# Performance work log

Hardware: AMD Instinct MI355X
Metric: run time of the kernel (lower is better)

The kernel has to match this reference:

```python
import jax, jax.numpy as jnp
import numpy as np

B, C, N = 16, 128, 2048  # batch, channels (SA_Layer(128)), num points


def setup_inputs() -> dict:
    key = jax.random.key(0)
    ks = jax.random.split(key, 6)
    x = jax.random.normal(ks[0], (B, C, N), jnp.float32)
    wq = jax.random.normal(ks[1], (C // 4, C), jnp.float32) * 0.05  # shared q/k 1x1 conv, no bias
    wv = jax.random.normal(ks[2], (C, C), jnp.float32) * 0.05
    bv = jax.random.normal(ks[3], (C,), jnp.float32) * 0.05
    wt = jax.random.normal(ks[4], (C, C), jnp.float32) * 0.05
    bt = jax.random.normal(ks[5], (C,), jnp.float32) * 0.05
    gamma = jnp.ones((C,), jnp.float32)   # BatchNorm1d weight
    beta = jnp.zeros((C,), jnp.float32)   # BatchNorm1d bias
    bn_mean = jnp.zeros((C,), jnp.float32)  # running mean (eval mode)
    bn_var = jnp.ones((C,), jnp.float32)    # running var (eval mode)
    return dict(x=x, wq=wq, wv=wv, bv=bv, wt=wt, bt=bt,
                gamma=gamma, beta=beta, bn_mean=bn_mean, bn_var=bn_var)


def reference(x, wq, wv, bv, wt, bt, gamma, beta, bn_mean, bn_var):
    EPS = 1e-9
    BN_EPS = 1e-5
    # q_conv and k_conv share weights (tied in __init__)
    x_q = jnp.einsum('dc,bcn->bnd', wq, x)               # [B, N, C/4]
    x_k = jnp.einsum('dc,bcn->bdn', wq, x)               # [B, C/4, N]
    energy = jnp.einsum('bnd,bdm->bnm', x_q, x_k)        # [B, N, N]
    attn = jax.nn.softmax(energy, axis=-1)
    # offset-attention renormalization: divide by column sum
    attn = attn / (EPS + attn.sum(axis=1, keepdims=True))
    x_v = jnp.einsum('dc,bcn->bdn', wv, x) + bv[None, :, None]   # [B, C, N]
    x_r = jnp.einsum('bdn,bnm->bdm', x_v, attn)                  # [B, C, N]
    t = jnp.einsum('dc,bcn->bdn', wt, x - x_r) + bt[None, :, None]
    # BatchNorm1d (eval mode) + ReLU
    t = (t - bn_mean[None, :, None]) * jax.lax.rsqrt(bn_var + BN_EPS)[None, :, None]
    t = t * gamma[None, :, None] + beta[None, :, None]
    return x + jax.nn.relu(t)
```

## Files before the change

kernel.cpp:

```cpp
#include <hip/hip_runtime.h>
#include <hip/hip_bf16.h>
#include <math.h>

#define BB 16
#define CC 128
#define NN 2048
#define CQ 32

typedef __attribute__((ext_vector_type(8))) short bf16x8;
typedef __attribute__((ext_vector_type(4))) float f32x4;
typedef __attribute__((ext_vector_type(16))) float f32x16;

__device__ __forceinline__ ushort f2b(float f) {
    __hip_bfloat16 h = __float2bfloat16(f);
    return *reinterpret_cast<ushort*>(&h);
}
__device__ __forceinline__ float b2f(ushort u) {
    union { unsigned u; float f; } v; v.u = ((unsigned)u) << 16;
    return v.f;
}
__device__ __forceinline__ bf16x8 as_b8(uint4 u) {
    union { uint4 u; bf16x8 b; } v; v.u = u; return v.b;
}
__device__ __forceinline__ float fexp2(float x) {
    return __builtin_amdgcn_exp2f(x);
}

#define OFF_VB  524288
#define OFF_XRB 2621440
#define OFF_RSI 4718592

#define QSCALE 1.2011224087864498f

__global__ __launch_bounds__(256) void k_proj(const float* __restrict__ x,
        const float* __restrict__ wq, const float* __restrict__ wv,
        const float* __restrict__ bv, ushort* __restrict__ Qt, ushort* __restrict__ Vb) {
    __shared__ ushort Wl[160][136];
    __shared__ ushort Xs[64][136];
    int bid = (blockIdx.x & 7) * 64 + (blockIdx.x >> 3);
    int b  = bid >> 5;
    int n0 = (bid & 31) << 6;
    int tid = threadIdx.x;
    #pragma unroll
    for (int k = 0; k < 20; ++k) {
        int idx = k * 256 + tid;
        int r = idx >> 5, c4 = (idx & 31) << 2;
        const float* srcw = (r < 32) ? (wq + r * 128 + c4) : (wv + (r - 32) * 128 + c4);
        float4 w4 = *(const float4*)srcw;
        float s = (r < 32) ? QSCALE : 1.0f;
        *(ushort4*)&Wl[r][c4] = make_ushort4(f2b(w4.x * s), f2b(w4.y * s),
                                             f2b(w4.z * s), f2b(w4.w * s));
    }
    const float* xb = x + (size_t)b * CC * NN;
    for (int idx = tid; idx < 2048; idx += 256) {
        int c = idx >> 4, n4 = (idx & 15) << 2;
        float4 xv = *(const float4*)&xb[c * NN + n0 + n4];
        Xs[n4][c]     = f2b(xv.x);
        Xs[n4 + 1][c] = f2b(xv.y);
        Xs[n4 + 2][c] = f2b(xv.z);
        Xs[n4 + 3][c] = f2b(xv.w);
    }
    __syncthreads();
    int w = tid >> 6, l = tid & 63, lr = l & 15, lg = l >> 4;
    f32x4 zero = {0.f, 0.f, 0.f, 0.f};
    int nn = n0 + w * 16 + lr;
    for (int dt = 0; dt < 10; ++dt) {
        f32x4 acc = zero;
        #pragma unroll
        for (int k = 0; k < 4; ++k) {
            bf16x8 a  = *(const bf16x8*)&Wl[dt * 16 + lr][k * 32 + lg * 8];
            bf16x8 bx = *(const bf16x8*)&Xs[w * 16 + lr][k * 32 + lg * 8];
            acc = __builtin_amdgcn_mfma_f32_16x16x32_bf16(a, bx, acc, 0, 0, 0);
        }
        if (dt < 2) {
            ushort4 p = make_ushort4(f2b(acc[0]), f2b(acc[1]), f2b(acc[2]), f2b(acc[3]));
            *(ushort4*)&Qt[(size_t)(b * NN + nn) * CQ + dt * 16 + lg * 4] = p;
        } else {
            #pragma unroll
            for (int i = 0; i < 4; ++i) {
                int vd = (dt - 2) * 16 + lg * 4 + i;
                Vb[(size_t)(b * CC + vd) * NN + nn] = f2b(acc[i] + bv[vd]);
            }
        }
    }
}

__global__ __launch_bounds__(512) void k_rowstats(const ushort* __restrict__ Qt,
        float* __restrict__ RSI) {
    __shared__ ushort Qm[128][36];
    __shared__ float Sred[2][64];
    int bid = (blockIdx.x & 7) * 64 + (blockIdx.x >> 3);
    int b  = bid >> 5;
    int n0 = (bid & 31) << 6;
    int tid = threadIdx.x;
    int w = tid >> 6, l = tid & 63, lr = l & 15, lg = l >> 4;
    int wn = w & 3, wm = w >> 2;
    const ushort* Qtb = Qt + (size_t)b * NN * CQ;
    bf16x8 aq = *(const bf16x8*)&Qtb[(size_t)(n0 + wn * 16 + lr) * CQ + lg * 8];
    int sr = tid >> 2, sc = (tid & 3) * 8;
    uint4 q0 = *(const uint4*)&Qtb[(size_t)sr * CQ + sc];
    float S[4] = {0.f, 0.f, 0.f, 0.f};
    f32x4 zero = {0.f, 0.f, 0.f, 0.f};
    for (int t = 0; t < 16; ++t) {
        __syncthreads();
        *(uint4*)&Qm[sr][sc] = q0;
        __syncthreads();
        if (t < 15)
            q0 = *(const uint4*)&Qtb[(size_t)((t + 1) * 128 + sr) * CQ + sc];
        #pragma unroll
        for (int mi = 0; mi < 4; ++mi) {
            bf16x8 bq = *(const bf16x8*)&Qm[(wm * 4 + mi) * 16 + lr][lg * 8];
            f32x4 e = __builtin_amdgcn_mfma_f32_16x16x32_bf16(aq, bq, zero, 0, 0, 0);
            S[0] += fexp2(e[0]); S[1] += fexp2(e[1]);
            S[2] += fexp2(e[2]); S[3] += fexp2(e[3]);
        }
    }
    #pragma unroll
    for (int d = 1; d < 16; d <<= 1) {
        #pragma unroll
        for (int i = 0; i < 4; ++i) S[i] += __shfl_xor(S[i], d);
    }
    if (lr == 0) {
        #pragma unroll
        for (int i = 0; i < 4; ++i) Sred[wm][wn * 16 + lg * 4 + i] = S[i];
    }
    __syncthreads();
    if (tid < 64)
        RSI[b * NN + n0 + tid] = 1.f / (Sred[0][tid] + Sred[1][tid]);
}

__global__ __launch_bounds__(768, 3) void k_attn_pv(const ushort* __restrict__ Qt,
        const ushort* __restrict__ Vb, const float* __restrict__ RSI,
        ushort* __restrict__ XRb) {
    __shared__ ushort Vs[2][128][68];
    __shared__ ushort Ws[2][128][68];
    __shared__ float csred[4][128];
    __shared__ float csum[128];
    int bid = (blockIdx.x & 7) * 32 + (blockIdx.x >> 3);
    int b  = bid >> 4;
    int m0 = (bid & 15) << 7;
    int tid = threadIdx.x;
    int w = tid >> 6, l = tid & 63, lr = l & 15, lg = l >> 4;
    const ushort* Qtb = Qt + (size_t)b * NN * CQ;
    const ushort* Vbb = Vb + (size_t)b * CC * NN;
    const float*  RSb = RSI + (size_t)b * NN;
    f32x4 zero = {0.f, 0.f, 0.f, 0.f};
    bool producer = (w < 8);

    int wn = w & 3, mh = w >> 2;
    bf16x8 bm[4];
    float cs[4] = {0.f, 0.f, 0.f, 0.f};
    int sv = 0, shv = 0;
    const ushort* vsrc = nullptr;
    bf16x8 aq_nx; float4 rsi_nx;
    int cw = w - 8;
    int dh = cw >> 1, mh2 = cw & 1;
    int ar = l & 31, kh = l >> 5;
    f32x16 pacc00, pacc01, pacc10, pacc11;

    if (producer) {
        #pragma unroll
        for (int mi = 0; mi < 4; ++mi)
            bm[mi] = *(const bf16x8*)&Qtb[(size_t)(m0 + (mh * 4 + mi) * 16 + lr) * CQ + lg * 8];
        sv = tid >> 2; shv = (tid & 3) * 16;
        vsrc = Vbb + (size_t)sv * NN + shv;
        {
            uint4 v0 = *(const uint4*)(vsrc);
            uint4 v1 = *(const uint4*)(vsrc + 8);
            ushort* dst = &Vs[0][sv][shv];
            *(uint2*)(dst)      = make_uint2(v0.x, v0.y);
            *(uint2*)(dst + 4)  = make_uint2(v0.z, v0.w);
            *(uint2*)(dst + 8)  = make_uint2(v1.x, v1.y);
            *(uint2*)(dst + 12) = make_uint2(v1.z, v1.w);
        }
        {
            bf16x8 aq0 = *(const bf16x8*)&Qtb[(size_t)(wn * 16 + lr) * CQ + lg * 8];
            float4 r4 = *(const float4*)&RSb[wn * 16 + lg * 4];
            int nb = wn * 16 + lg * 4;
            #pragma unroll
            for (int mi = 0; mi < 4; ++mi) {
                f32x4 e = __builtin_amdgcn_mfma_f32_16x16x32_bf16(aq0, bm[mi], zero, 0, 0, 0);
                float w0 = fexp2(e[0]) * r4.x;
                float w1 = fexp2(e[1]) * r4.y;
                float w2 = fexp2(e[2]) * r4.z;
                float w3 = fexp2(e[3]) * r4.w;
                cs[mi] += w0 + w1 + w2 + w3;
                *(ushort4*)&Ws[0][(mh * 4 + mi) * 16 + lr][nb] =
                    make_ushort4(f2b(w0), f2b(w1), f2b(w2), f2b(w3));
            }
        }
        aq_nx  = *(const bf16x8*)&Qtb[(size_t)(64 + wn * 16 + lr) * CQ + lg * 8];
        rsi_nx = *(const float4*)&RSb[64 + wn * 16 + lg * 4];
    } else {
        #pragma unroll
        for (int r = 0; r < 16; ++r) {
            pacc00[r] = 0.f; pacc01[r] = 0.f; pacc10[r] = 0.f; pacc11[r] = 0.f;
        }
    }
    __syncthreads();
    for (int t = 0; t < 32; ++t) {
        int cur = t & 1;
        if (producer) {
            if (t < 31) {
                int ntn = (t + 1) * 64;
                uint4 v0 = *(const uint4*)(vsrc + ntn);
                uint4 v1 = *(const uint4*)(vsrc + ntn + 8);
                bf16x8 aq = aq_nx;
                float4 r4 = rsi_nx;
                if (t < 30) {
                    int nt2 = (t + 2) * 64;
                    aq_nx  = *(const bf16x8*)&Qtb[(size_t)(nt2 + wn * 16 + lr) * CQ + lg * 8];
                    rsi_nx = *(const float4*)&RSb[nt2 + wn * 16 + lg * 4];
                }
                int nb = wn * 16 + lg * 4;
                #pragma unroll
                for (int mi = 0; mi < 4; ++mi) {
                    f32x4 e = __builtin_amdgcn_mfma_f32_16x16x32_bf16(aq, bm[mi], zero, 0, 0, 0);
                    float w0 = fexp2(e[0]) * r4.x;
                    float w1 = fexp2(e[1]) * r4.y;
                    float w2 = fexp2(e[2]) * r4.z;
                    float w3 = fexp2(e[3]) * r4.w;
                    cs[mi] += w0 + w1 + w2 + w3;
                    *(ushort4*)&Ws[cur ^ 1][(mh * 4 + mi) * 16 + lr][nb] =
                        make_ushort4(f2b(w0), f2b(w1), f2b(w2), f2b(w3));
                }
                ushort* dst = &Vs[cur ^ 1][sv][shv];
                *(uint2*)(dst)      = make_uint2(v0.x, v0.y);
                *(uint2*)(dst + 4)  = make_uint2(v0.z, v0.w);
                *(uint2*)(dst + 8)  = make_uint2(v1.x, v1.y);
                *(uint2*)(dst + 12) = make_uint2(v1.z, v1.w);
            }
        } else {
            __builtin_amdgcn_s_setprio(1);
            #pragma unroll
            for (int kk = 0; kk < 4; ++kk) {
                const ushort* vp0 = &Vs[cur][dh * 64 + ar][kk * 16 + kh * 8];
                const ushort* vp1 = &Vs[cur][dh * 64 + 32 + ar][kk * 16 + kh * 8];
                uint2 a0 = *(const uint2*)vp0; uint2 a1 = *(const uint2*)(vp0 + 4);
                uint2 a2 = *(const uint2*)vp1; uint2 a3 = *(const uint2*)(vp1 + 4);
                bf16x8 va0 = as_b8(make_uint4(a0.x, a0.y, a1.x, a1.y));
                bf16x8 va1 = as_b8(make_uint4(a2.x, a2.y, a3.x, a3.y));
                const ushort* wp0 = &Ws[cur][mh2 * 64 + ar][kk * 16 + kh * 8];
                const ushort* wp1 = &Ws[cur][mh2 * 64 + 32 + ar][kk * 16 + kh * 8];
                uint2 b0 = *(const uint2*)wp0; uint2 b1 = *(const uint2*)(wp0 + 4);
                uint2 c0 = *(const uint2*)wp1; uint2 c1 = *(const uint2*)(wp1 + 4);
                bf16x8 wb0 = as_b8(make_uint4(b0.x, b0.y, b1.x, b1.y));
                bf16x8 wb1 = as_b8(make_uint4(c0.x, c0.y, c1.x, c1.y));
                pacc00 = __builtin_amdgcn_mfma_f32_32x32x16_bf16(va0, wb0, pacc00, 0, 0, 0);
                pacc01 = __builtin_amdgcn_mfma_f32_32x32x16_bf16(va0, wb1, pacc01, 0, 0, 0);
                pacc10 = __builtin_amdgcn_mfma_f32_32x32x16_bf16(va1, wb0, pacc10, 0, 0, 0);
                pacc11 = __builtin_amdgcn_mfma_f32_32x32x16_bf16(va1, wb1, pacc11, 0, 0, 0);
            }
            __builtin_amdgcn_s_setprio(0);
        }
        __syncthreads();
    }
    if (producer) {
        #pragma unroll
        for (int mi = 0; mi < 4; ++mi) {
            cs[mi] += __shfl_xor(cs[mi], 16);
            cs[mi] += __shfl_xor(cs[mi], 32);
        }
        if (lg == 0) {
            #pragma unroll
            for (int mi = 0; mi < 4; ++mi)
                csred[wn][(mh * 4 + mi) * 16 + lr] = cs[mi];
        }
    }
    __syncthreads();
    if (tid < 128) {
        float tot = csred[0][tid] + csred[1][tid] + csred[2][tid] + csred[3][tid];
        csum[tid] = 1.f / (1e-9f + tot);
    }
    __syncthreads();
    if (!producer) {
        float inv0 = csum[mh2 * 64 + ar];
        float inv1 = csum[mh2 * 64 + 32 + ar];
        int mA = m0 + mh2 * 64 + ar;
        #pragma unroll
        for (int r = 0; r < 16; ++r) {
            int d0 = dh * 64 + (r & 3) + 8 * (r >> 2) + 4 * kh;
            XRb[(size_t)(b * CC + d0) * NN + mA]          = f2b(pacc00[r] * inv0);
            XRb[(size_t)(b * CC + d0) * NN + mA + 32]     = f2b(pacc01[r] * inv1);
            XRb[(size_t)(b * CC + d0 + 32) * NN + mA]      = f2b(pacc10[r] * inv0);
            XRb[(size_t)(b * CC + d0 + 32) * NN + mA + 32] = f2b(pacc11[r] * inv1);
        }
    }
}

__global__ __launch_bounds__(256) void k_final(const float* __restrict__ x,
        const ushort* __restrict__ XRb, const float* __restrict__ wt,
        const float* __restrict__ bt, const float* __restrict__ gamma,
        const float* __restrict__ beta, const float* __restrict__ bn_mean,
        const float* __restrict__ bn_var, float* __restrict__ out) {
    __shared__ ushort Wl[128][136];
    __shared__ ushort Us[64][136];
    __shared__ float fAl[128], fBl[128];
    int bid = (blockIdx.x & 7) * 64 + (blockIdx.x >> 3);
    int b  = bid >> 5;
    int n0 = (bid & 31) << 6;
    int tid = threadIdx.x;
    #pragma unroll
    for (int k = 0; k < 16; ++k) {
        int idx = k * 256 + tid;
        int r = idx >> 5, c4 = (idx & 31) << 2;
        float4 w4 = *(const float4*)&wt[r * 128 + c4];
        *(ushort4*)&Wl[r][c4] = make_ushort4(f2b(w4.x), f2b(w4.y), f2b(w4.z), f2b(w4.w));
    }
    if (tid < 128) {
        float A = gamma[tid] * rsqrtf(bn_var[tid] + 1e-5f);
        fAl[tid] = A;
        fBl[tid] = (bt[tid] - bn_mean[tid]) * A + beta[tid];
    }
    const float*  xb  = x   + (size_t)b * CC * NN;
    const ushort* xrb = XRb + (size_t)b * CC * NN;
    for (int idx = tid; idx < 2048; idx += 256) {
        int c = idx >> 4, n4 = (idx & 15) << 2;
        float4 xv = *(const float4*)&xb[c * NN + n0 + n4];
        ushort4 rv = *(const ushort4*)&xrb[c * NN + n0 + n4];
        Us[n4][c]     = f2b(xv.x - b2f(rv.x));
        Us[n4 + 1][c] = f2b(xv.y - b2f(rv.y));
        Us[n4 + 2][c] = f2b(xv.z - b2f(rv.z));
        Us[n4 + 3][c] = f2b(xv.w - b2f(rv.w));
    }
    __syncthreads();
    int w = tid >> 6, l = tid & 63, lr = l & 15, lg = l >> 4;
    f32x4 zero = {0.f, 0.f, 0.f, 0.f};
    int nn = n0 + w * 16 + lr;
    for (int dt = 0; dt < 8; ++dt) {
        f32x4 acc = zero;
        #pragma unroll
        for (int k = 0; k < 4; ++k) {
            bf16x8 a  = *(const bf16x8*)&Wl[dt * 16 + lr][k * 32 + lg * 8];
            bf16x8 bx = *(const bf16x8*)&Us[w * 16 + lr][k * 32 + lg * 8];
            acc = __builtin_amdgcn_mfma_f32_16x16x32_bf16(a, bx, acc, 0, 0, 0);
        }
        #pragma unroll
        for (int i = 0; i < 4; ++i) {
            int r = dt * 16 + lg * 4 + i;
            float t = acc[i] * fAl[r] + fBl[r];
            t = fmaxf(t, 0.f);
            out[(size_t)(b * CC + r) * NN + nn] = xb[r * NN + nn] + t;
        }
    }
}

extern "C" void kernel_launch(void* const* d_in, const int* in_sizes, int n_in,
                              void* d_out, int out_size, void* d_ws, size_t ws_size,
                              hipStream_t stream) {
    const float* x       = (const float*)d_in[0];
    const float* wq      = (const float*)d_in[1];
    const float* wv      = (const float*)d_in[2];
    const float* bv      = (const float*)d_in[3];
    const float* wt      = (const float*)d_in[4];
    const float* bt      = (const float*)d_in[5];
    const float* gamma   = (const float*)d_in[6];
    const float* beta    = (const float*)d_in[7];
    const float* bn_mean = (const float*)d_in[8];
    const float* bn_var  = (const float*)d_in[9];
    float* out = (float*)d_out;
    float* ws  = (float*)d_ws;

    ushort* Qt   = (ushort*)ws;
    ushort* Vbp  = (ushort*)(ws + OFF_VB);
    ushort* XRb  = (ushort*)(ws + OFF_XRB);
    float*  RSI  = ws + OFF_RSI;

    k_proj<<<BB * 32, 256, 0, stream>>>(x, wq, wv, bv, Qt, Vbp);
    k_rowstats<<<BB * 32, 512, 0, stream>>>(Qt, RSI);
    k_attn_pv<<<BB * 16, 768, 0, stream>>>(Qt, Vbp, RSI, XRb);
    k_final<<<BB * 32, 256, 0, stream>>>(x, XRb, wt, bt, gamma, beta, bn_mean, bn_var, out);
}
```

Measured before the change: 66.98 us.

## Fuse final transform, BatchNorm and residual into attention PV kernel

Removes the separate final kernel and the bf16 XR intermediate buffer. The attention kernel now computes x - x_r in shared memory (reusing the V staging buffer) and runs the wt matmul with BatchNorm, ReLU and the residual add in its epilogue. This saves one launch and a full global round trip of the intermediate. In exchange it adds LDS for the wt weights, tail work in which only 4 of the 12 waves get a second tile, and possibly lower occupancy for the large attention kernel.

```diff
diff --git a/kernel.cpp b/kernel.cpp
--- a/kernel.cpp
+++ b/kernel.cpp
@@ -22,12 +22,14 @@
 __device__ __forceinline__ bf16x8 as_b8(uint4 u) {
     union { uint4 u; bf16x8 b; } v; v.u = u; return v.b;
 }
+__device__ __forceinline__ bf16x8 as_b8_2(uint2 a, uint2 b) {
+    return as_b8(make_uint4(a.x, a.y, b.x, b.y));
+}
 __device__ __forceinline__ float fexp2(float x) {
     return __builtin_amdgcn_exp2f(x);
 }
 
 #define OFF_VB  524288
-#define OFF_XRB 2621440
 #define OFF_RSI 4718592
 
 #define QSCALE 1.2011224087864498f
@@ -131,11 +133,16 @@
 
 __global__ __launch_bounds__(768, 3) void k_attn_pv(const ushort* __restrict__ Qt,
         const ushort* __restrict__ Vb, const float* __restrict__ RSI,
-        ushort* __restrict__ XRb) {
+        const float* __restrict__ x, const float* __restrict__ wt,
+        const float* __restrict__ bt, const float* __restrict__ gamma,
+        const float* __restrict__ beta, const float* __restrict__ bn_mean,
+        const float* __restrict__ bn_var, float* __restrict__ out) {
     __shared__ ushort Vs[2][128][68];
     __shared__ ushort Ws[2][128][68];
+    __shared__ ushort wtl[16896];
     __shared__ float csred[4][128];
     __shared__ float csum[128];
+    __shared__ float fAl[128], fBl[128];
     int bid = (blockIdx.x & 7) * 32 + (blockIdx.x >> 3);
     int b  = bid >> 4;
     int m0 = (bid & 15) << 7;
@@ -144,8 +151,22 @@
     const ushort* Qtb = Qt + (size_t)b * NN * CQ;
     const ushort* Vbb = Vb + (size_t)b * CC * NN;
     const float*  RSb = RSI + (size_t)b * NN;
+    const float*  xb  = x   + (size_t)b * CC * NN;
+    float*        outb = out + (size_t)b * CC * NN;
     f32x4 zero = {0.f, 0.f, 0.f, 0.f};
     bool producer = (w < 8);
+
+    for (int idx = tid; idx < 4096; idx += 768) {
+        int r = idx >> 5, c4 = (idx & 31) << 2;
+        float4 w4 = *(const float4*)&wt[r * 128 + c4];
+        *(ushort4*)&wtl[r * 132 + c4] =
+            make_ushort4(f2b(w4.x), f2b(w4.y), f2b(w4.z), f2b(w4.w));
+    }
+    if (tid < 128) {
+        float A = gamma[tid] * rsqrtf(bn_var[tid] + 1e-5f);
+        fAl[tid] = A;
+        fBl[tid] = (bt[tid] - bn_mean[tid]) * A + beta[tid];
+    }
 
     int wn = w & 3, mh = w >> 2;
     bf16x8 bm[4];
@@ -238,14 +259,14 @@
                 const ushort* vp1 = &Vs[cur][dh * 64 + 32 + ar][kk * 16 + kh * 8];
                 uint2 a0 = *(const uint2*)vp0; uint2 a1 = *(const uint2*)(vp0 + 4);
                 uint2 a2 = *(const uint2*)vp1; uint2 a3 = *(const uint2*)(vp1 + 4);
-                bf16x8 va0 = as_b8(make_uint4(a0.x, a0.y, a1.x, a1.y));
-                bf16x8 va1 = as_b8(make_uint4(a2.x, a2.y, a3.x, a3.y));
+                bf16x8 va0 = as_b8_2(a0, a1);
+                bf16x8 va1 = as_b8_2(a2, a3);
                 const ushort* wp0 = &Ws[cur][mh2 * 64 + ar][kk * 16 + kh * 8];
                 const ushort* wp1 = &Ws[cur][mh2 * 64 + 32 + ar][kk * 16 + kh * 8];
                 uint2 b0 = *(const uint2*)wp0; uint2 b1 = *(const uint2*)(wp0 + 4);
                 uint2 c0 = *(const uint2*)wp1; uint2 c1 = *(const uint2*)(wp1 + 4);
-                bf16x8 wb0 = as_b8(make_uint4(b0.x, b0.y, b1.x, b1.y));
-                bf16x8 wb1 = as_b8(make_uint4(c0.x, c0.y, c1.x, c1.y));
+                bf16x8 wb0 = as_b8_2(b0, b1);
+                bf16x8 wb1 = as_b8_2(c0, c1);
                 pacc00 = __builtin_amdgcn_mfma_f32_32x32x16_bf16(va0, wb0, pacc00, 0, 0, 0);
                 pacc01 = __builtin_amdgcn_mfma_f32_32x32x16_bf16(va0, wb1, pacc01, 0, 0, 0);
                 pacc10 = __builtin_amdgcn_mfma_f32_32x32x16_bf16(va1, wb0, pacc10, 0, 0, 0);
@@ -273,74 +294,59 @@
         csum[tid] = 1.f / (1e-9f + tot);
     }
     __syncthreads();
+    ushort* UsP = &Vs[0][0][0];
     if (!producer) {
         float inv0 = csum[mh2 * 64 + ar];
         float inv1 = csum[mh2 * 64 + 32 + ar];
         int mA = m0 + mh2 * 64 + ar;
-        #pragma unroll
-        for (int r = 0; r < 16; ++r) {
-            int d0 = dh * 64 + (r & 3) + 8 * (r >> 2) + 4 * kh;
-            XRb[(size_t)(b * CC + d0) * NN + mA]          = f2b(pacc00[r] * inv0);
-            XRb[(size_t)(b * CC + d0) * NN + mA + 32]     = f2b(pacc01[r] * inv1);
-            XRb[(size_t)(b * CC + d0 + 32) * NN + mA]      = f2b(pacc10[r] * inv0);
-            XRb[(size_t)(b * CC + d0 + 32) * NN + mA + 32] = f2b(pacc11[r] * inv1);
-        }
-    }
-}
-
-__global__ __launch_bounds__(256) void k_final(const float* __restrict__ x,
-        const ushort* __restrict__ XRb, const float* __restrict__ wt,
-        const float* __restrict__ bt, const float* __restrict__ gamma,
-        const float* __restrict__ beta, const float* __restrict__ bn_mean,
-        const float* __restrict__ bn_var, float* __restrict__ out) {
-    __shared__ ushort Wl[128][136];
-    __shared__ ushort Us[64][136];
-    __shared__ float fAl[128], fBl[128];
-    int bid = (blockIdx.x & 7) * 64 + (blockIdx.x >> 3);
-    int b  = bid >> 5;
-    int n0 = (bid & 31) << 6;
-    int tid = threadIdx.x;
-    #pragma unroll
-    for (int k = 0; k < 16; ++k) {
-        int idx = k * 256 + tid;
-        int r = idx >> 5, c4 = (idx & 31) << 2;
-        float4 w4 = *(const float4*)&wt[r * 128 + c4];
-        *(ushort4*)&Wl[r][c4] = make_ushort4(f2b(w4.x), f2b(w4.y), f2b(w4.z), f2b(w4.w));
-    }
-    if (tid < 128) {
-        float A = gamma[tid] * rsqrtf(bn_var[tid] + 1e-5f);
-        fAl[tid] = A;
-        fBl[tid] = (bt[tid] - bn_mean[tid]) * A + beta[tid];
-    }
-    const float*  xb  = x   + (size_t)b * CC * NN;
-    const ushort* xrb = XRb + (size_t)b * CC * NN;
-    for (int idx = tid; idx < 2048; idx += 256) {
-        int c = idx >> 4, n4 = (idx & 15) << 2;
-        float4 xv = *(const float4*)&xb[c * NN + n0 + n4];
-        ushort4 rv = *(const ushort4*)&xrb[c * NN + n0 + n4];
-        Us[n4][c]     = f2b(xv.x - b2f(rv.x));
-        Us[n4 + 1][c] = f2b(xv.y - b2f(rv.y));
-        Us[n4 + 2][c] = f2b(xv.z - b2f(rv.z));
-        Us[n4 + 3][c] = f2b(xv.w - b2f(rv.w));
-    }
-    __syncthreads();
-    int w = tid >> 6, l = tid & 63, lr = l & 15, lg = l >> 4;
-    f32x4 zero = {0.f, 0.f, 0.f, 0.f};
-    int nn = n0 + w * 16 + lr;
-    for (int dt = 0; dt < 8; ++dt) {
-        f32x4 acc = zero;
-        #pragma unroll
-        for (int k = 0; k < 4; ++k) {
-            bf16x8 a  = *(const bf16x8*)&Wl[dt * 16 + lr][k * 32 + lg * 8];
-            bf16x8 bx = *(const bf16x8*)&Us[w * 16 + lr][k * 32 + lg * 8];
-            acc = __builtin_amdgcn_mfma_f32_16x16x32_bf16(a, bx, acc, 0, 0, 0);
-        }
-        #pragma unroll
-        for (int i = 0; i < 4; ++i) {
-            int r = dt * 16 + lg * 4 + i;
-            float t = acc[i] * fAl[r] + fBl[r];
-            t = fmaxf(t, 0.f);
-            out[(size_t)(b * CC + r) * NN + nn] = xb[r * NN + nn] + t;
+        int mL = mh2 * 64 + ar;
+        #pragma unroll
+        for (int g = 0; g < 4; ++g) {
+            int db = dh * 64 + 8 * g + 4 * kh;
+            ushort4 u00, u01, u10, u11;
+            #pragma unroll
+            for (int j = 0; j < 4; ++j) {
+                int r = 4 * g + j;
+                float x00 = xb[(size_t)(db + j) * NN + mA];
+                float x01 = xb[(size_t)(db + j) * NN + mA + 32];
+                float x10 = xb[(size_t)(db + 32 + j) * NN + mA];
+                float x11 = xb[(size_t)(db + 32 + j) * NN + mA + 32];
+                ((ushort*)&u00)[j] = f2b(x00 - pacc00[r] * inv0);
+                ((ushort*)&u01)[j] = f2b(x01 - pacc01[r] * inv1);
+                ((ushort*)&u10)[j] = f2b(x10 - pacc10[r] * inv0);
+                ((ushort*)&u11)[j] = f2b(x11 - pacc11[r] * inv1);
+            }
+            *(ushort4*)&UsP[mL * 132 + db]             = u00;
+            *(ushort4*)&UsP[(mL + 32) * 132 + db]      = u01;
+            *(ushort4*)&UsP[mL * 132 + db + 32]        = u10;
+            *(ushort4*)&UsP[(mL + 32) * 132 + db + 32] = u11;
+        }
+    }
+    __syncthreads();
+    for (int tile = w; tile < 16; tile += 12) {
+        int rt = tile >> 2, mt = tile & 3;
+        f32x16 acc;
+        #pragma unroll
+        for (int r = 0; r < 16; ++r) acc[r] = 0.f;
+        #pragma unroll
+        for (int kk = 0; kk < 8; ++kk) {
+            const ushort* ap = &wtl[(rt * 32 + ar) * 132 + kk * 16 + kh * 8];
+            uint2 a0 = *(const uint2*)ap; uint2 a1 = *(const uint2*)(ap + 4);
+            const ushort* bp = &UsP[(mt * 32 + ar) * 132 + kk * 16 + kh * 8];
+            uint2 b0 = *(const uint2*)bp; uint2 b1 = *(const uint2*)(bp + 4);
+            acc = __builtin_amdgcn_mfma_f32_32x32x16_bf16(
+                as_b8_2(a0, a1), as_b8_2(b0, b1), acc, 0, 0, 0);
+        }
+        int m = m0 + mt * 32 + ar;
+        #pragma unroll
+        for (int g = 0; g < 4; ++g) {
+            #pragma unroll
+            for (int j = 0; j < 4; ++j) {
+                int r = rt * 32 + j + 8 * g + 4 * kh;
+                float t = acc[4 * g + j] * fAl[r] + fBl[r];
+                t = fmaxf(t, 0.f);
+                outb[(size_t)r * NN + m] = xb[(size_t)r * NN + m] + t;
+            }
         }
     }
 }
@@ -363,11 +369,10 @@
 
     ushort* Qt   = (ushort*)ws;
     ushort* Vbp  = (ushort*)(ws + OFF_VB);
-    ushort* XRb  = (ushort*)(ws + OFF_XRB);
     float*  RSI  = ws + OFF_RSI;
 
     k_proj<<<BB * 32, 256, 0, stream>>>(x, wq, wv, bv, Qt, Vbp);
     k_rowstats<<<BB * 32, 512, 0, stream>>>(Qt, RSI);
-    k_attn_pv<<<BB * 16, 768, 0, stream>>>(Qt, Vbp, RSI, XRb);
-    k_final<<<BB * 32, 256, 0, stream>>>(x, XRb, wt, bt, gamma, beta, bn_mean, bn_var, out);
-}
+    k_attn_pv<<<BB * 16, 768, 0, stream>>>(Qt, Vbp, RSI, x, wt, bt, gamma, beta,
+                                           bn_mean, bn_var, out);
+}
```

Result: faster. 62.50 us (-6.7%).
